# Kernel optimization log

Hardware: AMD Instinct MI355X
Metric: run time of the kernel (lower is better)

## Reference

```python
import jax, jax.numpy as jnp
import numpy as np
from jax import lax

H, H2, VJ, VC = 512, 256, 70, 2000
B, LIN, T = 64, 1024, 256
START = 1  # char2index['<s>']


def gru_step(h, x, Wih, Whh, bih, bhh):
    # PyTorch GRU cell math; gates ordered (r, z, n)
    gi = x @ Wih.T + bih
    gh = h @ Whh.T + bhh
    ir, iz, inn = jnp.split(gi, 3, axis=-1)
    hr, hz, hn = jnp.split(gh, 3, axis=-1)
    r = jax.nn.sigmoid(ir + hr)
    z = jax.nn.sigmoid(iz + hz)
    n = jnp.tanh(inn + r * hn)
    return (1.0 - z) * n + z * h


def setup_inputs() -> dict:
    key = jax.random.key(0)
    ks = jax.random.split(key, 24)
    u = lambda k, s: jax.random.uniform(k, s, jnp.float32, -0.1, 0.1)
    return {
        "input_tokens": jax.random.randint(ks[0], (B, LIN), 0, VJ),
        "target_tokens": jax.random.randint(ks[1], (B, T), 0, VC),
        "loss_mask": jnp.ones((B, T), jnp.float32),
        "emb_jamo": u(ks[2], (VJ, H)),
        "emb_char": u(ks[3], (VC, H)),
        "enc_Wih_f": u(ks[4], (3 * H2, H)),  "enc_Whh_f": u(ks[5], (3 * H2, H2)),
        "enc_bih_f": u(ks[6], (3 * H2,)),    "enc_bhh_f": u(ks[7], (3 * H2,)),
        "enc_Wih_b": u(ks[8], (3 * H2, H)),  "enc_Whh_b": u(ks[9], (3 * H2, H2)),
        "enc_bih_b": u(ks[10], (3 * H2,)),   "enc_bhh_b": u(ks[11], (3 * H2,)),
        "dec_Wih": u(ks[12], (3 * H, H)),    "dec_Whh": u(ks[13], (3 * H, H)),
        "dec_bih": u(ks[14], (3 * H,)),      "dec_bhh": u(ks[15], (3 * H,)),
        "attn_W": u(ks[16], (H, 2 * H)),     "attn_b": u(ks[17], (H,)),
        "comb_W": u(ks[18], (H, 2 * H)),     "comb_b": u(ks[19], (H,)),
        "out_W": u(ks[20], (VC, H)),         "out_b": u(ks[21], (VC,)),
    }


def reference(input_tokens, target_tokens, loss_mask, emb_jamo, emb_char,
              enc_Wih_f, enc_Whh_f, enc_bih_f, enc_bhh_f,
              enc_Wih_b, enc_Whh_b, enc_bih_b, enc_bhh_b,
              dec_Wih, dec_Whh, dec_bih, dec_bhh,
              attn_W, attn_b, comb_W, comb_b, out_W, out_b):
    b, lin = input_tokens.shape
    t_len = target_tokens.shape[1]
    h2 = enc_Whh_f.shape[1]

    # --- Encoder: step-by-step bidirectional GRU (per original Python loop,
    # both directions advance forward in time since seq_len=1 per call) ---
    xs = jnp.swapaxes(emb_jamo[input_tokens], 0, 1)  # [Lin, B, H]

    def enc_step(carry, xt):
        hf, hb = carry
        hf = gru_step(hf, xt, enc_Wih_f, enc_Whh_f, enc_bih_f, enc_bhh_f)
        hb = gru_step(hb, xt, enc_Wih_b, enc_Whh_b, enc_bih_b, enc_bhh_b)
        return (hf, hb), jnp.concatenate([hf, hb], axis=-1)

    init = (jnp.zeros((b, h2), xs.dtype), jnp.zeros((b, h2), xs.dtype))
    _, enc_out_t = lax.scan(enc_step, init, xs)      # [Lin, B, H]
    enc_out = jnp.swapaxes(enc_out_t, 0, 1)          # [B, Lin, H]
    h0 = enc_out_t[-1]                               # decoder init hidden [B, H]

    # --- Decoder: attention + GRU, greedy argmax feedback ---
    tok0 = jnp.full((b,), START, dtype=input_tokens.dtype)

    def dec_step(carry, _):
        tok, h = carry
        emb = emb_char[tok]                                           # [B, H]
        key_ = jnp.concatenate([emb, h], -1) @ attn_W.T + attn_b      # [B, H]
        scores = jnp.einsum('blh,bh->bl', enc_out, key_)              # [B, Lin]
        w = jax.nn.softmax(scores, axis=1)
        ctx = jnp.einsum('bl,blh->bh', w, enc_out)                    # [B, H]
        g = jax.nn.relu(jnp.concatenate([emb, ctx], -1) @ comb_W.T + comb_b)
        h_new = gru_step(h, g, dec_Wih, dec_Whh, dec_bih, dec_bhh)
        logp = jax.nn.log_softmax(h_new @ out_W.T + out_b, axis=-1)   # [B, VC]
        nxt = jnp.argmax(logp, axis=-1).astype(tok.dtype)
        return (nxt, h_new), (logp, w)

    _, (logps, ws) = lax.scan(dec_step, (tok0, h0), None, length=t_len)
    decoder_outputs = jnp.swapaxes(logps, 0, 1)       # [B, T, VC]
    decoder_attentions = jnp.transpose(ws, (1, 2, 0)) # [B, Lin, T]

    # NLLLoss(reduction='none') masked, mean over batch, summed over steps, /T
    nll = -jnp.take_along_axis(decoder_outputs, target_tokens[..., None], axis=-1)[..., 0]
    loss = jnp.sum(jnp.mean(nll * loss_mask, axis=0)) / t_len
    return decoder_outputs, decoder_attentions, loss
```

## Files before the change

### kernel.cpp

```cpp
#include <hip/hip_runtime.h>
#include <hip/hip_bf16.h>
#include <cstdint>
#include <cstddef>


#define DEV __device__ __forceinline__

constexpr int kH = 512, kH2 = 256, kVC = 2000, kB = 64, kLIN = 1024, kT = 256;
constexpr int kSTART = 1;

__global__ __launch_bounds__(256) void k_zero(float* p, int n) {
  int i = blockIdx.x * 256 + threadIdx.x;
  if (i < n) p[i] = 0.f;
}

__global__ __launch_bounds__(256)
void k_gi_table(const float* emb_jamo, const float* Wf, const float* Wb,
                const float* bihf, const float* bihb, float* gi) {
  int v = blockIdx.x >> 1, d = blockIdx.x & 1;
  const float* W = d ? Wb : Wf;
  const float* bih = d ? bihb : bihf;
  __shared__ float x[kH];
  for (int k = threadIdx.x; k < kH; k += 256) x[k] = emb_jamo[v * kH + k];
  __syncthreads();
  for (int j = threadIdx.x; j < 3 * kH2; j += 256) {
    float acc = bih[j];
    const float* row = W + (size_t)j * kH;
    for (int k = 0; k < kH; k += 4) {
      float4 f = *(const float4*)(row + k);
      acc += x[k] * f.x + x[k + 1] * f.y + x[k + 2] * f.z + x[k + 3] * f.w;
    }
    gi[(size_t)(v * 2 + d) * 768 + j] = acc;
  }
}

__global__ __launch_bounds__(256)
void k_ac_emb(const float* emb_char, const float* attn_W, const float* attn_b,
              const float* comb_W, const float* comb_b, float* A, float* C) {
  int v = blockIdx.x;
  __shared__ float x[kH];
  for (int k = threadIdx.x; k < kH; k += 256) x[k] = emb_char[v * kH + k];
  __syncthreads();
  for (int j = threadIdx.x; j < kH; j += 256) {
    float a = attn_b[j], c = comb_b[j];
    const float* ra = attn_W + (size_t)j * 1024;
    const float* rc = comb_W + (size_t)j * 1024;
    for (int k = 0; k < kH; k += 4) {
      float4 fa = *(const float4*)(ra + k), fc = *(const float4*)(rc + k);
      a += x[k] * fa.x + x[k + 1] * fa.y + x[k + 2] * fa.z + x[k + 3] * fa.w;
      c += x[k] * fc.x + x[k + 1] * fc.y + x[k + 2] * fc.z + x[k + 3] * fc.w;
    }
    A[(size_t)v * kH + j] = a;
    C[(size_t)v * kH + j] = c;
  }
}

__global__ __launch_bounds__(256)
void k_enc_step(const int* tokens, const float* Whf, const float* Whb,
                const float* bhhf, const float* bhhb, const float* gi,
                float* henc, float* enc, int t, int pp, int BC, int lbc, int b0) {
  int d = blockIdx.x >> lbc;
  int blk = blockIdx.x & (BC - 1);
  int b = threadIdx.x & (BC - 1), q = threadIdx.x >> lbc;
  int u = blk * (256 >> lbc) + q;
  const float* Whh = d ? Whb : Whf;
  const float* bhh = d ? bhhb : bhhf;
  const float* hin = henc + (size_t)(pp * 2 + d) * kH2 * BC;
  float* hout = henc + (size_t)((1 - pp) * 2 + d) * kH2 * BC;

  const float* wr = Whh + (size_t)(0 * kH2 + u) * kH2;
  const float* wz = Whh + (size_t)(1 * kH2 + u) * kH2;
  const float* wn = Whh + (size_t)(2 * kH2 + u) * kH2;
  float ar = bhh[u], az = bhh[kH2 + u], an = bhh[2 * kH2 + u];
  for (int k = 0; k < kH2; k += 4) {
    float4 fr = *(const float4*)(wr + k);
    float4 fz = *(const float4*)(wz + k);
    float4 fn = *(const float4*)(wn + k);
    float h0v = hin[(k + 0) * BC + b], h1v = hin[(k + 1) * BC + b];
    float h2v = hin[(k + 2) * BC + b], h3v = hin[(k + 3) * BC + b];
    ar += h0v * fr.x + h1v * fr.y + h2v * fr.z + h3v * fr.w;
    az += h0v * fz.x + h1v * fz.y + h2v * fz.z + h3v * fz.w;
    an += h0v * fn.x + h1v * fn.y + h2v * fn.z + h3v * fn.w;
  }
  int v = tokens[(size_t)(b0 + b) * kLIN + t];
  const float* git = gi + (size_t)(v * 2 + d) * 768;
  float r = 1.f / (1.f + expf(-(git[u] + ar)));
  float z = 1.f / (1.f + expf(-(git[kH2 + u] + az)));
  float n = tanhf(git[2 * kH2 + u] + r * an);
  float hprev = hin[u * BC + b];
  float hnew = (1.f - z) * n + z * hprev;
  hout[u * BC + b] = hnew;
  enc[((size_t)b * kLIN + t) * kH + d * kH2 + u] = hnew;
}

__global__ __launch_bounds__(256)
void k_prologue(const float* enc, const float* Atab, const float* aW,
                float* hr, float* ht, float* key, int* tok, int BC) {
  int b = blockIdx.x, tid = threadIdx.x;
  __shared__ float h[kH];
  const float* h0 = enc + ((size_t)b * kLIN + (kLIN - 1)) * kH;
  for (int k = tid; k < kH; k += 256) {
    float v = h0[k];
    h[k] = v;
    hr[(size_t)b * kH + k] = v;
    ht[(size_t)k * BC + b] = v;
  }
  if (tid == 0) tok[b] = kSTART;
  __syncthreads();
  const float* A = Atab + (size_t)kSTART * kH;
  for (int j = tid; j < kH; j += 256) {
    const float* row = aW + (size_t)j * 1024 + 512;
    float acc = A[j];
    for (int k = 0; k < kH; k += 4) {
      float4 f = *(const float4*)(row + k);
      acc += h[k] * f.x + h[k + 1] * f.y + h[k + 2] * f.z + h[k + 3] * f.w;
    }
    key[(size_t)b * kH + j] = acc;
  }
}

__global__ __launch_bounds__(256)
void k_scores(const float* encAll, const float* keyAll, float* sc,
              float* pm, float* pd, float* pctx) {
  int b = blockIdx.x >> 3, lt = blockIdx.x & 7;
  int tid = threadIdx.x, lane = tid & 63, w = tid >> 6, hl = lane & 31, half = lane >> 5;
  __shared__ float s_tile[128], e_tile[128], red[128];
  const float* enc = encAll + (size_t)b * kLIN * kH;
  float kreg[16];
  const float* key = keyAll + (size_t)b * kH + hl * 16;
#pragma unroll
  for (int m = 0; m < 16; m += 4) *(float4*)(kreg + m) = *(const float4*)(key + m);
  for (int i = 0; i < 16; i++) {
    int ll = w * 32 + i * 2 + half;
    int l = lt * 128 + ll;
    const float* row = enc + (size_t)l * kH + hl * 16;
    float acc = 0.f;
#pragma unroll
    for (int m = 0; m < 16; m += 4) {
      float4 v = *(const float4*)(row + m);
      acc += v.x * kreg[m] + v.y * kreg[m + 1] + v.z * kreg[m + 2] + v.w * kreg[m + 3];
    }
#pragma unroll
    for (int m2 = 16; m2 > 0; m2 >>= 1) acc += __shfl_xor(acc, m2, 32);
    if (hl == 0) { s_tile[ll] = acc; sc[(size_t)b * kLIN + l] = acc; }
  }
  __syncthreads();
  if (tid < 128) red[tid] = s_tile[tid];
  __syncthreads();
  for (int s = 64; s > 0; s >>= 1) {
    if (tid < s) red[tid] = fmaxf(red[tid], red[tid + s]);
    __syncthreads();
  }
  float mt = red[0];
  __syncthreads();
  if (tid < 128) { e_tile[tid] = expf(s_tile[tid] - mt); red[tid] = e_tile[tid]; }
  __syncthreads();
  for (int s = 64; s > 0; s >>= 1) {
    if (tid < s) red[tid] += red[tid + s];
    __syncthreads();
  }
  float dt = red[0];
  int h0i = tid * 2;
  float cx = 0.f, cy = 0.f;
  const float* base = enc + (size_t)(lt * 128) * kH + h0i;
  for (int l = 0; l < 128; l++) {
    float e = e_tile[l];
    float2 v = *(const float2*)(base + (size_t)l * kH);
    cx += e * v.x; cy += e * v.y;
  }
  float* pc = pctx + ((size_t)b * 8 + lt) * kH;
  pc[h0i] = cx; pc[h0i + 1] = cy;
  if (tid == 0) { pm[b * 8 + lt] = mt; pd[b * 8 + lt] = dt; }
}

__global__ __launch_bounds__(256)
void k_ctx_g(const float* cW, const float* Ctab, const float* sc,
             const float* pm, const float* pd, const float* pctx,
             const int* tok, float* out1, float* gt, int BC, int b0, int t) {
  int b = blockIdx.x, tid = threadIdx.x;
  __shared__ float f8[8], MD[2], ctxl[kH];
  __shared__ int tokl;
  if (tid == 0) {
    float M = -1e30f;
    for (int i = 0; i < 8; i++) M = fmaxf(M, pm[b * 8 + i]);
    float D = 0.f;
    for (int i = 0; i < 8; i++) {
      float f = expf(pm[b * 8 + i] - M);
      f8[i] = f; D += f * pd[b * 8 + i];
    }
    MD[0] = M; MD[1] = 1.f / D;
    tokl = tok[b];
  }
  __syncthreads();
  float M = MD[0], invD = MD[1];
  int h0i = tid * 2;
  float cx = 0.f, cy = 0.f;
  for (int i = 0; i < 8; i++) {
    const float* pc = pctx + ((size_t)b * 8 + i) * kH + h0i;
    cx += f8[i] * pc[0]; cy += f8[i] * pc[1];
  }
  ctxl[h0i] = cx * invD; ctxl[h0i + 1] = cy * invD;
  int gb = b0 + b;
  for (int l = tid; l < kLIN; l += 256)
    out1[((size_t)gb * kLIN + l) * kT + t] = expf(sc[(size_t)b * kLIN + l] - M) * invD;
  __syncthreads();
  int tk = tokl;
  for (int j = tid; j < kH; j += 256) {
    const float* row = cW + (size_t)j * 1024 + 512;
    float acc = Ctab[(size_t)tk * kH + j];
    for (int k = 0; k < kH; k += 4) {
      float4 f = *(const float4*)(row + k);
      acc += ctxl[k] * f.x + ctxl[k + 1] * f.y + ctxl[k + 2] * f.z + ctxl[k + 3] * f.w;
    }
    gt[(size_t)j * BC + b] = fmaxf(acc, 0.f);
  }
}

__global__ __launch_bounds__(256)
void k_gru(const float* Wih, const float* Whh, const float* bih, const float* bhh,
           const float* gt, float* ht, float* hr, int BC, int lbc, int pp) {
  int tid = threadIdx.x;
  int b = tid & (BC - 1), q = tid >> lbc;
  int u = blockIdx.x * (256 >> lbc) + q;
  const float* htp = ht + (size_t)pp * kH * BC;
  float air = bih[u], aiz = bih[kH + u], ain = bih[2 * kH + u];
  float ahr = bhh[u], ahz = bhh[kH + u], ahn = bhh[2 * kH + u];
  const float* wir = Wih + (size_t)(0 * kH + u) * kH;
  const float* wiz = Wih + (size_t)(1 * kH + u) * kH;
  const float* win = Wih + (size_t)(2 * kH + u) * kH;
  const float* whr = Whh + (size_t)(0 * kH + u) * kH;
  const float* whz = Whh + (size_t)(1 * kH + u) * kH;
  const float* whn = Whh + (size_t)(2 * kH + u) * kH;
  for (int k = 0; k < kH; k += 4) {
    float4 fir = *(const float4*)(wir + k), fiz = *(const float4*)(wiz + k), fin = *(const float4*)(win + k);
    float4 fhr = *(const float4*)(whr + k), fhz = *(const float4*)(whz + k), fhn = *(const float4*)(whn + k);
    float g0 = gt[(k + 0) * BC + b], g1 = gt[(k + 1) * BC + b];
    float g2 = gt[(k + 2) * BC + b], g3 = gt[(k + 3) * BC + b];
    float h0v = htp[(k + 0) * BC + b], h1v = htp[(k + 1) * BC + b];
    float h2v = htp[(k + 2) * BC + b], h3v = htp[(k + 3) * BC + b];
    air += g0 * fir.x + g1 * fir.y + g2 * fir.z + g3 * fir.w;
    aiz += g0 * fiz.x + g1 * fiz.y + g2 * fiz.z + g3 * fiz.w;
    ain += g0 * fin.x + g1 * fin.y + g2 * fin.z + g3 * fin.w;
    ahr += h0v * fhr.x + h1v * fhr.y + h2v * fhr.z + h3v * fhr.w;
    ahz += h0v * fhz.x + h1v * fhz.y + h2v * fhz.z + h3v * fhz.w;
    ahn += h0v * fhn.x + h1v * fhn.y + h2v * fhn.z + h3v * fhn.w;
  }
  float r = 1.f / (1.f + expf(-(air + ahr)));
  float z = 1.f / (1.f + expf(-(aiz + ahz)));
  float n = tanhf(ain + r * ahn);
  float hp = htp[(size_t)u * BC + b];
  float hnew = (1.f - z) * n + z * hp;
  ht[(size_t)(1 - pp) * kH * BC + (size_t)u * BC + b] = hnew;
  hr[(size_t)(1 - pp) * BC * kH + (size_t)b * kH + u] = hnew;
}

__global__ __launch_bounds__(256)
void k_logits(const float* oW, const float* ob, const float* hr, float* lg,
              int BC, int np) {
  int b = blockIdx.x >> 3, ct = blockIdx.x & 7;
  int tid = threadIdx.x, lane = tid & 63, w = tid >> 6, hl = lane & 31, half = lane >> 5;
  const float* hrow = hr + (size_t)np * BC * kH + (size_t)b * kH + hl * 16;
  float hreg[16];
#pragma unroll
  for (int m = 0; m < 16; m += 4) *(float4*)(hreg + m) = *(const float4*)(hrow + m);
  int c0 = ct * 250;
  for (int i = 0; i < 32; i++) {
    int c = c0 + i * 8 + w * 2 + half;
    if (c < c0 + 250) {
      const float* row = oW + (size_t)c * kH + hl * 16;
      float acc = 0.f;
#pragma unroll
      for (int m = 0; m < 16; m += 4) {
        float4 v = *(const float4*)(row + m);
        acc += v.x * hreg[m] + v.y * hreg[m + 1] + v.z * hreg[m + 2] + v.w * hreg[m + 3];
      }
#pragma unroll
      for (int m2 = 16; m2 > 0; m2 >>= 1) acc += __shfl_xor(acc, m2, 32);
      if (hl == 0) lg[(size_t)b * kVC + c] = acc + ob[c];
    }
  }
}

__global__ __launch_bounds__(256)
void k_finish(const float* aW, const int* targets, const float* mask,
              const float* Atab, const float* hr, const float* lg,
              float* key, int* tok, float* loss, float* out0,
              int BC, int b0, int t, int np) {
  int b = blockIdx.x, tid = threadIdx.x, gb = b0 + b;
  __shared__ float rv[256]; __shared__ int ri[256]; __shared__ float rs[256];
  __shared__ float hsh[kH];
  const float* lrow = lg + (size_t)b * kVC;
  float xv[8];
  float bv = -3.4e38f; int bi = kVC;
#pragma unroll
  for (int i = 0; i < 8; i++) {
    int c = tid + i * 256;
    float x = (c < kVC) ? lrow[c] : -3.4e38f;
    xv[i] = x;
    if (x > bv) { bv = x; bi = c; }
  }
  rv[tid] = bv; ri[tid] = bi;
  __syncthreads();
  for (int s = 128; s > 0; s >>= 1) {
    if (tid < s) {
      float v2 = rv[tid + s]; int i2 = ri[tid + s];
      if (v2 > rv[tid] || (v2 == rv[tid] && i2 < ri[tid])) { rv[tid] = v2; ri[tid] = i2; }
    }
    __syncthreads();
  }
  float M = rv[0]; int nt = ri[0];
  float se = 0.f;
#pragma unroll
  for (int i = 0; i < 8; i++) { int c = tid + i * 256; if (c < kVC) se += expf(xv[i] - M); }
  rs[tid] = se;
  __syncthreads();
  for (int s = 128; s > 0; s >>= 1) {
    if (tid < s) rs[tid] += rs[tid + s];
    __syncthreads();
  }
  float lse = M + logf(rs[0]);
  float* orow = out0 + ((size_t)gb * kT + t) * kVC;
#pragma unroll
  for (int i = 0; i < 8; i++) { int c = tid + i * 256; if (c < kVC) orow[c] = xv[i] - lse; }
  if (tid == 0) {
    tok[b] = nt;
    int tg = targets[(size_t)gb * kT + t];
    float mk = mask[(size_t)gb * kT + t];
    atomicAdd(loss, (lse - lrow[tg]) * mk * (1.f / 16384.f));
  }
  const float* hrow = hr + (size_t)np * BC * kH + (size_t)b * kH;
  for (int k = tid; k < kH; k += 256) hsh[k] = hrow[k];
  __syncthreads();
  const float* A = Atab + (size_t)nt * kH;
  for (int j = tid; j < kH; j += 256) {
    const float* row = aW + (size_t)j * 1024 + 512;
    float acc = A[j];
    for (int k = 0; k < kH; k += 4) {
      float4 f = *(const float4*)(row + k);
      acc += hsh[k] * f.x + hsh[k + 1] * f.y + hsh[k + 2] * f.z + hsh[k + 3] * f.w;
    }
    key[(size_t)b * kH + j] = acc;
  }
}

__global__ void k_loss_out(float* dst, const float* loss) {
  if (threadIdx.x == 0 && blockIdx.x == 0) *dst = *loss;
}

extern "C" void kernel_launch(void* const* d_in, const int* in_sizes, int n_in,
                              void* d_out, int out_size, void* d_ws, size_t ws_size,
                              hipStream_t stream) {
  (void)in_sizes; (void)n_in;
  const int*   tok_in = (const int*)d_in[0];
  const int*   tgt    = (const int*)d_in[1];
  const float* mask   = (const float*)d_in[2];
  const float* emb_j  = (const float*)d_in[3];
  const float* emb_c  = (const float*)d_in[4];
  const float* eWif   = (const float*)d_in[5];
  const float* eWhf   = (const float*)d_in[6];
  const float* ebif   = (const float*)d_in[7];
  const float* ebhf   = (const float*)d_in[8];
  const float* eWib   = (const float*)d_in[9];
  const float* eWhb   = (const float*)d_in[10];
  const float* ebib   = (const float*)d_in[11];
  const float* ebhb   = (const float*)d_in[12];
  const float* dWi    = (const float*)d_in[13];
  const float* dWh    = (const float*)d_in[14];
  const float* dbi    = (const float*)d_in[15];
  const float* dbh    = (const float*)d_in[16];
  const float* aW     = (const float*)d_in[17];
  const float* ab     = (const float*)d_in[18];
  const float* cW     = (const float*)d_in[19];
  const float* cb     = (const float*)d_in[20];
  const float* oW     = (const float*)d_in[21];
  const float* ob     = (const float*)d_in[22];
  float* ws   = (float*)d_ws;
  float* out0 = (float*)d_out;
  float* out1 = out0 + (size_t)kB * kT * kVC;

  const size_t GI = 0;
  const size_t A  = GI + 107520;
  const size_t C  = A + 1024000;
  const size_t SMALL = C + 1024000;
  size_t o = SMALL;
  const size_t HENC = o; o += 4 * 256 * 64;
  const size_t KEY  = o; o += 64 * 512;
  const size_t SC   = o; o += 64 * 1024;
  const size_t PM   = o; o += 512;
  const size_t PD   = o; o += 512;
  const size_t PCT  = o; o += 64 * 8 * 512;
  const size_t GT   = o; o += 512 * 64;
  const size_t HR   = o; o += 2 * 64 * 512;
  const size_t HT   = o; o += 2 * 512 * 64;
  const size_t LG   = o; o += 64 * 2000;
  const size_t TOKo = o; o += 64;
  const size_t LOSS = o; o += 1;
  const size_t ENC  = o;
  const int small_n = (int)(ENC - SMALL);

  int BC = 64;
  while (BC > 8 && (ENC + (size_t)BC * kLIN * kH) * sizeof(float) > ws_size) BC >>= 1;
  int lbc = (BC == 64) ? 6 : (BC == 32) ? 5 : (BC == 16) ? 4 : 3;
  int NC = kB / BC;
  int* tokp = (int*)(ws + TOKo);

  k_zero<<<(small_n + 255) / 256, 256, 0, stream>>>(ws + SMALL, small_n);
  k_gi_table<<<140, 256, 0, stream>>>(emb_j, eWif, eWib, ebif, ebib, ws + GI);
  k_ac_emb<<<2000, 256, 0, stream>>>(emb_c, aW, ab, cW, cb, ws + A, ws + C);

  for (int c = 0; c < NC; c++) {
    int b0 = c * BC;
    k_zero<<<(4 * 256 * BC + 255) / 256, 256, 0, stream>>>(ws + HENC, 4 * 256 * BC);
    for (int t = 0; t < kLIN; t++)
      k_enc_step<<<2 * BC, 256, 0, stream>>>(tok_in, eWhf, eWhb, ebhf, ebhb,
                                             ws + GI, ws + HENC, ws + ENC,
                                             t, t & 1, BC, lbc, b0);
    k_prologue<<<BC, 256, 0, stream>>>(ws + ENC, ws + A, aW, ws + HR, ws + HT,
                                       ws + KEY, tokp, BC);
    for (int t = 0; t < kT; t++) {
      int pp = t & 1, np = 1 - pp;
      k_scores<<<BC * 8, 256, 0, stream>>>(ws + ENC, ws + KEY, ws + SC,
                                           ws + PM, ws + PD, ws + PCT);
      k_ctx_g<<<BC, 256, 0, stream>>>(cW, ws + C, ws + SC, ws + PM, ws + PD,
                                      ws + PCT, tokp, out1, ws + GT, BC, b0, t);
      k_gru<<<2 * BC, 256, 0, stream>>>(dWi, dWh, dbi, dbh, ws + GT,
                                        ws + HT, ws + HR, BC, lbc, pp);
      k_logits<<<BC * 8, 256, 0, stream>>>(oW, ob, ws + HR, ws + LG, BC, np);
      k_finish<<<BC, 256, 0, stream>>>(aW, tgt, mask, ws + A, ws + HR, ws + LG,
                                       ws + KEY, tokp, ws + LOSS, out0,
                                       BC, b0, t, np);
    }
  }
  k_loss_out<<<1, 64, 0, stream>>>(out0 + (size_t)out_size - 1, ws + LOSS);
}
```

Baseline: 62.72 ms.

## Fuse encoder and decoder time loops into persistent per-sequence kernels

The per-timestep launches (1024 encoder steps plus 5 kernels per decoder step) are replaced by two persistent kernels. The encoder runs one block per sequence and direction, looping over time with its hidden state in shared memory. The decoder runs one 1024-thread block per sequence that does scores, context, GRU, logits, log-softmax and key update inside the block. This removes thousands of launches and the global round-trips for intermediates. In exchange it uses far fewer blocks (only 2*BC or BC), so each block re-streams the weight matrices on its own and parallelism per step drops.

```diff
diff --git a/kernel.cpp b/kernel.cpp
--- a/kernel.cpp
+++ b/kernel.cpp
@@ -1,10 +1,7 @@
 #include <hip/hip_runtime.h>
-#include <hip/hip_bf16.h>
 #include <cstdint>
 #include <cstddef>
 
-
-#define DEV __device__ __forceinline__
 
 constexpr int kH = 512, kH2 = 256, kVC = 2000, kB = 64, kLIN = 1024, kT = 256;
 constexpr int kSTART = 1;
@@ -56,290 +53,308 @@
 }
 
 __global__ __launch_bounds__(256)
-void k_enc_step(const int* tokens, const float* Whf, const float* Whb,
-                const float* bhhf, const float* bhhb, const float* gi,
-                float* henc, float* enc, int t, int pp, int BC, int lbc, int b0) {
-  int d = blockIdx.x >> lbc;
-  int blk = blockIdx.x & (BC - 1);
-  int b = threadIdx.x & (BC - 1), q = threadIdx.x >> lbc;
-  int u = blk * (256 >> lbc) + q;
+void k_enc_pb(const int* tokens, const float* Whf, const float* Whb,
+              const float* bhhf, const float* bhhb, const float* gi,
+              float* enc, int b0) {
+  int b = blockIdx.x >> 1, d = blockIdx.x & 1;
+  int u = threadIdx.x;
   const float* Whh = d ? Whb : Whf;
   const float* bhh = d ? bhhb : bhhf;
-  const float* hin = henc + (size_t)(pp * 2 + d) * kH2 * BC;
-  float* hout = henc + (size_t)((1 - pp) * 2 + d) * kH2 * BC;
-
+  __shared__ float hsh[kH2];
+  hsh[u] = 0.f;
+  __syncthreads();
   const float* wr = Whh + (size_t)(0 * kH2 + u) * kH2;
   const float* wz = Whh + (size_t)(1 * kH2 + u) * kH2;
   const float* wn = Whh + (size_t)(2 * kH2 + u) * kH2;
-  float ar = bhh[u], az = bhh[kH2 + u], an = bhh[2 * kH2 + u];
-  for (int k = 0; k < kH2; k += 4) {
-    float4 fr = *(const float4*)(wr + k);
-    float4 fz = *(const float4*)(wz + k);
-    float4 fn = *(const float4*)(wn + k);
-    float h0v = hin[(k + 0) * BC + b], h1v = hin[(k + 1) * BC + b];
-    float h2v = hin[(k + 2) * BC + b], h3v = hin[(k + 3) * BC + b];
-    ar += h0v * fr.x + h1v * fr.y + h2v * fr.z + h3v * fr.w;
-    az += h0v * fz.x + h1v * fz.y + h2v * fz.z + h3v * fz.w;
-    an += h0v * fn.x + h1v * fn.y + h2v * fn.z + h3v * fn.w;
-  }
-  int v = tokens[(size_t)(b0 + b) * kLIN + t];
-  const float* git = gi + (size_t)(v * 2 + d) * 768;
-  float r = 1.f / (1.f + expf(-(git[u] + ar)));
-  float z = 1.f / (1.f + expf(-(git[kH2 + u] + az)));
-  float n = tanhf(git[2 * kH2 + u] + r * an);
-  float hprev = hin[u * BC + b];
-  float hnew = (1.f - z) * n + z * hprev;
-  hout[u * BC + b] = hnew;
-  enc[((size_t)b * kLIN + t) * kH + d * kH2 + u] = hnew;
-}
-
-__global__ __launch_bounds__(256)
-void k_prologue(const float* enc, const float* Atab, const float* aW,
-                float* hr, float* ht, float* key, int* tok, int BC) {
-  int b = blockIdx.x, tid = threadIdx.x;
-  __shared__ float h[kH];
-  const float* h0 = enc + ((size_t)b * kLIN + (kLIN - 1)) * kH;
-  for (int k = tid; k < kH; k += 256) {
-    float v = h0[k];
-    h[k] = v;
-    hr[(size_t)b * kH + k] = v;
-    ht[(size_t)k * BC + b] = v;
-  }
-  if (tid == 0) tok[b] = kSTART;
+  float br = bhh[u], bz = bhh[kH2 + u], bn = bhh[2 * kH2 + u];
+  const int* myTok = tokens + (size_t)(b0 + b) * kLIN;
+  float* encCol = enc + (size_t)b * kLIN * kH + d * kH2 + u;
+  for (int t = 0; t < kLIN; ++t) {
+    float ar = br, az = bz, an = bn;
+    for (int k = 0; k < kH2; k += 4) {
+      float4 fr = *(const float4*)(wr + k);
+      float4 fz = *(const float4*)(wz + k);
+      float4 fn = *(const float4*)(wn + k);
+      float h0v = hsh[k], h1v = hsh[k + 1], h2v = hsh[k + 2], h3v = hsh[k + 3];
+      ar += h0v * fr.x + h1v * fr.y + h2v * fr.z + h3v * fr.w;
+      az += h0v * fz.x + h1v * fz.y + h2v * fz.z + h3v * fz.w;
+      an += h0v * fn.x + h1v * fn.y + h2v * fn.z + h3v * fn.w;
+    }
+    int v = myTok[t];
+    const float* git = gi + (size_t)(v * 2 + d) * 768;
+    float r = 1.f / (1.f + expf(-(git[u] + ar)));
+    float z = 1.f / (1.f + expf(-(git[kH2 + u] + az)));
+    float n = tanhf(git[2 * kH2 + u] + r * an);
+    float hprev = hsh[u];
+    float hnew = (1.f - z) * n + z * hprev;
+    __syncthreads();
+    hsh[u] = hnew;
+    encCol[(size_t)t * kH] = hnew;
+    __syncthreads();
+  }
+}
+
+__global__ __launch_bounds__(1024, 1)
+void k_dec_pb(const float* encAll, const float* cW, const float* Ctab,
+              const float* dWi, const float* dWh, const float* dbi, const float* dbh,
+              const float* oW, const float* ob, const float* aW, const float* Atab,
+              const int* targets, const float* maskp,
+              float* loss, float* out0, float* out1, int b0) {
+  int b = blockIdx.x;
+  int tid = threadIdx.x;
+  int sg = tid >> 8, stid = tid & 255;
+  int lane = stid & 63, w = stid >> 6, hl = lane & 31, half = lane >> 5;
+
+  __shared__ float s_tile[4][128], e_tile[4][128], red[4][128];
+  __shared__ float pm_s[8], pd_s[8];
+  __shared__ float pctx_s[8][kH];
+  __shared__ __align__(16) float sc_all[kLIN];
+  __shared__ __align__(16) float key_s[kH];
+  __shared__ __align__(16) float hbuf[2][kH];
+  __shared__ __align__(16) float ctxl[kH];
+  __shared__ __align__(16) float gt_s[kH];
+  __shared__ float lg_s[kVC];
+  __shared__ float rv[256]; __shared__ int ri[256]; __shared__ float rs[256];
+  __shared__ float MD[2]; __shared__ float f8[8];
+  __shared__ int tok_s;
+
+  const float* encB = encAll + (size_t)b * kLIN * kH;
+  int gb = b0 + b;
+
+  for (int k = tid; k < kH; k += 1024) hbuf[0][k] = encB[(size_t)(kLIN - 1) * kH + k];
+  if (tid == 0) tok_s = kSTART;
   __syncthreads();
-  const float* A = Atab + (size_t)kSTART * kH;
-  for (int j = tid; j < kH; j += 256) {
+  if (tid < kH) {
+    int j = tid;
     const float* row = aW + (size_t)j * 1024 + 512;
-    float acc = A[j];
+    float acc = Atab[(size_t)kSTART * kH + j];
     for (int k = 0; k < kH; k += 4) {
       float4 f = *(const float4*)(row + k);
-      acc += h[k] * f.x + h[k + 1] * f.y + h[k + 2] * f.z + h[k + 3] * f.w;
-    }
-    key[(size_t)b * kH + j] = acc;
-  }
-}
-
-__global__ __launch_bounds__(256)
-void k_scores(const float* encAll, const float* keyAll, float* sc,
-              float* pm, float* pd, float* pctx) {
-  int b = blockIdx.x >> 3, lt = blockIdx.x & 7;
-  int tid = threadIdx.x, lane = tid & 63, w = tid >> 6, hl = lane & 31, half = lane >> 5;
-  __shared__ float s_tile[128], e_tile[128], red[128];
-  const float* enc = encAll + (size_t)b * kLIN * kH;
-  float kreg[16];
-  const float* key = keyAll + (size_t)b * kH + hl * 16;
-#pragma unroll
-  for (int m = 0; m < 16; m += 4) *(float4*)(kreg + m) = *(const float4*)(key + m);
-  for (int i = 0; i < 16; i++) {
-    int ll = w * 32 + i * 2 + half;
-    int l = lt * 128 + ll;
-    const float* row = enc + (size_t)l * kH + hl * 16;
-    float acc = 0.f;
-#pragma unroll
-    for (int m = 0; m < 16; m += 4) {
-      float4 v = *(const float4*)(row + m);
-      acc += v.x * kreg[m] + v.y * kreg[m + 1] + v.z * kreg[m + 2] + v.w * kreg[m + 3];
-    }
-#pragma unroll
-    for (int m2 = 16; m2 > 0; m2 >>= 1) acc += __shfl_xor(acc, m2, 32);
-    if (hl == 0) { s_tile[ll] = acc; sc[(size_t)b * kLIN + l] = acc; }
+      acc += hbuf[0][k] * f.x + hbuf[0][k + 1] * f.y + hbuf[0][k + 2] * f.z + hbuf[0][k + 3] * f.w;
+    }
+    key_s[j] = acc;
   }
   __syncthreads();
-  if (tid < 128) red[tid] = s_tile[tid];
-  __syncthreads();
-  for (int s = 64; s > 0; s >>= 1) {
-    if (tid < s) red[tid] = fmaxf(red[tid], red[tid + s]);
-    __syncthreads();
-  }
-  float mt = red[0];
-  __syncthreads();
-  if (tid < 128) { e_tile[tid] = expf(s_tile[tid] - mt); red[tid] = e_tile[tid]; }
-  __syncthreads();
-  for (int s = 64; s > 0; s >>= 1) {
-    if (tid < s) red[tid] += red[tid + s];
-    __syncthreads();
-  }
-  float dt = red[0];
-  int h0i = tid * 2;
-  float cx = 0.f, cy = 0.f;
-  const float* base = enc + (size_t)(lt * 128) * kH + h0i;
-  for (int l = 0; l < 128; l++) {
-    float e = e_tile[l];
-    float2 v = *(const float2*)(base + (size_t)l * kH);
-    cx += e * v.x; cy += e * v.y;
-  }
-  float* pc = pctx + ((size_t)b * 8 + lt) * kH;
-  pc[h0i] = cx; pc[h0i + 1] = cy;
-  if (tid == 0) { pm[b * 8 + lt] = mt; pd[b * 8 + lt] = dt; }
-}
-
-__global__ __launch_bounds__(256)
-void k_ctx_g(const float* cW, const float* Ctab, const float* sc,
-             const float* pm, const float* pd, const float* pctx,
-             const int* tok, float* out1, float* gt, int BC, int b0, int t) {
-  int b = blockIdx.x, tid = threadIdx.x;
-  __shared__ float f8[8], MD[2], ctxl[kH];
-  __shared__ int tokl;
-  if (tid == 0) {
-    float M = -1e30f;
-    for (int i = 0; i < 8; i++) M = fmaxf(M, pm[b * 8 + i]);
-    float D = 0.f;
-    for (int i = 0; i < 8; i++) {
-      float f = expf(pm[b * 8 + i] - M);
-      f8[i] = f; D += f * pd[b * 8 + i];
-    }
-    MD[0] = M; MD[1] = 1.f / D;
-    tokl = tok[b];
-  }
-  __syncthreads();
-  float M = MD[0], invD = MD[1];
-  int h0i = tid * 2;
-  float cx = 0.f, cy = 0.f;
-  for (int i = 0; i < 8; i++) {
-    const float* pc = pctx + ((size_t)b * 8 + i) * kH + h0i;
-    cx += f8[i] * pc[0]; cy += f8[i] * pc[1];
-  }
-  ctxl[h0i] = cx * invD; ctxl[h0i + 1] = cy * invD;
-  int gb = b0 + b;
-  for (int l = tid; l < kLIN; l += 256)
-    out1[((size_t)gb * kLIN + l) * kT + t] = expf(sc[(size_t)b * kLIN + l] - M) * invD;
-  __syncthreads();
-  int tk = tokl;
-  for (int j = tid; j < kH; j += 256) {
-    const float* row = cW + (size_t)j * 1024 + 512;
-    float acc = Ctab[(size_t)tk * kH + j];
-    for (int k = 0; k < kH; k += 4) {
-      float4 f = *(const float4*)(row + k);
-      acc += ctxl[k] * f.x + ctxl[k + 1] * f.y + ctxl[k + 2] * f.z + ctxl[k + 3] * f.w;
-    }
-    gt[(size_t)j * BC + b] = fmaxf(acc, 0.f);
-  }
-}
-
-__global__ __launch_bounds__(256)
-void k_gru(const float* Wih, const float* Whh, const float* bih, const float* bhh,
-           const float* gt, float* ht, float* hr, int BC, int lbc, int pp) {
-  int tid = threadIdx.x;
-  int b = tid & (BC - 1), q = tid >> lbc;
-  int u = blockIdx.x * (256 >> lbc) + q;
-  const float* htp = ht + (size_t)pp * kH * BC;
-  float air = bih[u], aiz = bih[kH + u], ain = bih[2 * kH + u];
-  float ahr = bhh[u], ahz = bhh[kH + u], ahn = bhh[2 * kH + u];
-  const float* wir = Wih + (size_t)(0 * kH + u) * kH;
-  const float* wiz = Wih + (size_t)(1 * kH + u) * kH;
-  const float* win = Wih + (size_t)(2 * kH + u) * kH;
-  const float* whr = Whh + (size_t)(0 * kH + u) * kH;
-  const float* whz = Whh + (size_t)(1 * kH + u) * kH;
-  const float* whn = Whh + (size_t)(2 * kH + u) * kH;
-  for (int k = 0; k < kH; k += 4) {
-    float4 fir = *(const float4*)(wir + k), fiz = *(const float4*)(wiz + k), fin = *(const float4*)(win + k);
-    float4 fhr = *(const float4*)(whr + k), fhz = *(const float4*)(whz + k), fhn = *(const float4*)(whn + k);
-    float g0 = gt[(k + 0) * BC + b], g1 = gt[(k + 1) * BC + b];
-    float g2 = gt[(k + 2) * BC + b], g3 = gt[(k + 3) * BC + b];
-    float h0v = htp[(k + 0) * BC + b], h1v = htp[(k + 1) * BC + b];
-    float h2v = htp[(k + 2) * BC + b], h3v = htp[(k + 3) * BC + b];
-    air += g0 * fir.x + g1 * fir.y + g2 * fir.z + g3 * fir.w;
-    aiz += g0 * fiz.x + g1 * fiz.y + g2 * fiz.z + g3 * fiz.w;
-    ain += g0 * fin.x + g1 * fin.y + g2 * fin.z + g3 * fin.w;
-    ahr += h0v * fhr.x + h1v * fhr.y + h2v * fhr.z + h3v * fhr.w;
-    ahz += h0v * fhz.x + h1v * fhz.y + h2v * fhz.z + h3v * fhz.w;
-    ahn += h0v * fhn.x + h1v * fhn.y + h2v * fhn.z + h3v * fhn.w;
-  }
-  float r = 1.f / (1.f + expf(-(air + ahr)));
-  float z = 1.f / (1.f + expf(-(aiz + ahz)));
-  float n = tanhf(ain + r * ahn);
-  float hp = htp[(size_t)u * BC + b];
-  float hnew = (1.f - z) * n + z * hp;
-  ht[(size_t)(1 - pp) * kH * BC + (size_t)u * BC + b] = hnew;
-  hr[(size_t)(1 - pp) * BC * kH + (size_t)b * kH + u] = hnew;
-}
-
-__global__ __launch_bounds__(256)
-void k_logits(const float* oW, const float* ob, const float* hr, float* lg,
-              int BC, int np) {
-  int b = blockIdx.x >> 3, ct = blockIdx.x & 7;
-  int tid = threadIdx.x, lane = tid & 63, w = tid >> 6, hl = lane & 31, half = lane >> 5;
-  const float* hrow = hr + (size_t)np * BC * kH + (size_t)b * kH + hl * 16;
-  float hreg[16];
-#pragma unroll
-  for (int m = 0; m < 16; m += 4) *(float4*)(hreg + m) = *(const float4*)(hrow + m);
-  int c0 = ct * 250;
-  for (int i = 0; i < 32; i++) {
-    int c = c0 + i * 8 + w * 2 + half;
-    if (c < c0 + 250) {
-      const float* row = oW + (size_t)c * kH + hl * 16;
-      float acc = 0.f;
-#pragma unroll
-      for (int m = 0; m < 16; m += 4) {
-        float4 v = *(const float4*)(row + m);
-        acc += v.x * hreg[m] + v.y * hreg[m + 1] + v.z * hreg[m + 2] + v.w * hreg[m + 3];
-      }
-#pragma unroll
-      for (int m2 = 16; m2 > 0; m2 >>= 1) acc += __shfl_xor(acc, m2, 32);
-      if (hl == 0) lg[(size_t)b * kVC + c] = acc + ob[c];
-    }
-  }
-}
-
-__global__ __launch_bounds__(256)
-void k_finish(const float* aW, const int* targets, const float* mask,
-              const float* Atab, const float* hr, const float* lg,
-              float* key, int* tok, float* loss, float* out0,
-              int BC, int b0, int t, int np) {
-  int b = blockIdx.x, tid = threadIdx.x, gb = b0 + b;
-  __shared__ float rv[256]; __shared__ int ri[256]; __shared__ float rs[256];
-  __shared__ float hsh[kH];
-  const float* lrow = lg + (size_t)b * kVC;
-  float xv[8];
-  float bv = -3.4e38f; int bi = kVC;
-#pragma unroll
-  for (int i = 0; i < 8; i++) {
-    int c = tid + i * 256;
-    float x = (c < kVC) ? lrow[c] : -3.4e38f;
-    xv[i] = x;
-    if (x > bv) { bv = x; bi = c; }
-  }
-  rv[tid] = bv; ri[tid] = bi;
-  __syncthreads();
-  for (int s = 128; s > 0; s >>= 1) {
-    if (tid < s) {
-      float v2 = rv[tid + s]; int i2 = ri[tid + s];
-      if (v2 > rv[tid] || (v2 == rv[tid] && i2 < ri[tid])) { rv[tid] = v2; ri[tid] = i2; }
-    }
-    __syncthreads();
-  }
-  float M = rv[0]; int nt = ri[0];
-  float se = 0.f;
-#pragma unroll
-  for (int i = 0; i < 8; i++) { int c = tid + i * 256; if (c < kVC) se += expf(xv[i] - M); }
-  rs[tid] = se;
-  __syncthreads();
-  for (int s = 128; s > 0; s >>= 1) {
-    if (tid < s) rs[tid] += rs[tid + s];
-    __syncthreads();
-  }
-  float lse = M + logf(rs[0]);
-  float* orow = out0 + ((size_t)gb * kT + t) * kVC;
-#pragma unroll
-  for (int i = 0; i < 8; i++) { int c = tid + i * 256; if (c < kVC) orow[c] = xv[i] - lse; }
-  if (tid == 0) {
-    tok[b] = nt;
-    int tg = targets[(size_t)gb * kT + t];
-    float mk = mask[(size_t)gb * kT + t];
-    atomicAdd(loss, (lse - lrow[tg]) * mk * (1.f / 16384.f));
-  }
-  const float* hrow = hr + (size_t)np * BC * kH + (size_t)b * kH;
-  for (int k = tid; k < kH; k += 256) hsh[k] = hrow[k];
-  __syncthreads();
-  const float* A = Atab + (size_t)nt * kH;
-  for (int j = tid; j < kH; j += 256) {
-    const float* row = aW + (size_t)j * 1024 + 512;
-    float acc = A[j];
-    for (int k = 0; k < kH; k += 4) {
-      float4 f = *(const float4*)(row + k);
-      acc += hsh[k] * f.x + hsh[k + 1] * f.y + hsh[k + 2] * f.z + hsh[k + 3] * f.w;
-    }
-    key[(size_t)b * kH + j] = acc;
+
+  for (int t = 0; t < kT; ++t) {
+    int pp = t & 1;
+    const float* hprev = hbuf[pp];
+    float* hnew = hbuf[1 - pp];
+
+    float kreg[16];
+#pragma unroll
+    for (int m = 0; m < 16; m += 4) *(float4*)(kreg + m) = *(const float4*)(key_s + hl * 16 + m);
+    for (int r = 0; r < 2; ++r) {
+      int lt = sg + r * 4;
+      for (int i0 = 0; i0 < 16; i0 += 2) {
+        float4 v[2][4];
+#pragma unroll
+        for (int j = 0; j < 2; j++) {
+          int ll = w * 32 + (i0 + j) * 2 + half;
+          const float* row = encB + (size_t)(lt * 128 + ll) * kH + hl * 16;
+#pragma unroll
+          for (int m = 0; m < 4; m++) v[j][m] = *(const float4*)(row + m * 4);
+        }
+#pragma unroll
+        for (int j = 0; j < 2; j++) {
+          int ll = w * 32 + (i0 + j) * 2 + half;
+          float acc = 0.f;
+#pragma unroll
+          for (int m = 0; m < 4; m++)
+            acc += v[j][m].x * kreg[4 * m] + v[j][m].y * kreg[4 * m + 1] +
+                   v[j][m].z * kreg[4 * m + 2] + v[j][m].w * kreg[4 * m + 3];
+#pragma unroll
+          for (int m2 = 16; m2 > 0; m2 >>= 1) acc += __shfl_xor(acc, m2, 32);
+          if (hl == 0) { s_tile[sg][ll] = acc; sc_all[lt * 128 + ll] = acc; }
+        }
+      }
+      __syncthreads();
+      if (stid < 128) red[sg][stid] = s_tile[sg][stid];
+      __syncthreads();
+      for (int s = 64; s > 0; s >>= 1) {
+        if (stid < s) red[sg][stid] = fmaxf(red[sg][stid], red[sg][stid + s]);
+        __syncthreads();
+      }
+      float mt = red[sg][0];
+      __syncthreads();
+      if (stid < 128) { e_tile[sg][stid] = expf(s_tile[sg][stid] - mt); red[sg][stid] = e_tile[sg][stid]; }
+      __syncthreads();
+      for (int s = 64; s > 0; s >>= 1) {
+        if (stid < s) red[sg][stid] += red[sg][stid + s];
+        __syncthreads();
+      }
+      float dt = red[sg][0];
+      int h0i = stid * 2;
+      float cx = 0.f, cy = 0.f;
+      const float* base = encB + (size_t)(lt * 128) * kH + h0i;
+      for (int l0 = 0; l0 < 128; l0 += 4) {
+        float2 v0 = *(const float2*)(base + (size_t)(l0 + 0) * kH);
+        float2 v1 = *(const float2*)(base + (size_t)(l0 + 1) * kH);
+        float2 v2 = *(const float2*)(base + (size_t)(l0 + 2) * kH);
+        float2 v3 = *(const float2*)(base + (size_t)(l0 + 3) * kH);
+        float e0 = e_tile[sg][l0], e1 = e_tile[sg][l0 + 1];
+        float e2 = e_tile[sg][l0 + 2], e3 = e_tile[sg][l0 + 3];
+        cx += e0 * v0.x; cy += e0 * v0.y;
+        cx += e1 * v1.x; cy += e1 * v1.y;
+        cx += e2 * v2.x; cy += e2 * v2.y;
+        cx += e3 * v3.x; cy += e3 * v3.y;
+      }
+      pctx_s[lt][h0i] = cx; pctx_s[lt][h0i + 1] = cy;
+      if (stid == 0) { pm_s[lt] = mt; pd_s[lt] = dt; }
+      __syncthreads();
+    }
+
+    if (tid == 0) {
+      float M = -1e30f;
+      for (int i = 0; i < 8; i++) M = fmaxf(M, pm_s[i]);
+      float D = 0.f;
+      for (int i = 0; i < 8; i++) {
+        float f = expf(pm_s[i] - M);
+        f8[i] = f; D += f * pd_s[i];
+      }
+      MD[0] = M; MD[1] = 1.f / D;
+    }
+    __syncthreads();
+    float M = MD[0], invD = MD[1];
+    if (tid < 256) {
+      int h0i = tid * 2;
+      float cx = 0.f, cy = 0.f;
+      for (int i = 0; i < 8; i++) { cx += f8[i] * pctx_s[i][h0i]; cy += f8[i] * pctx_s[i][h0i + 1]; }
+      ctxl[h0i] = cx * invD; ctxl[h0i + 1] = cy * invD;
+    }
+    out1[((size_t)gb * kLIN + tid) * kT + t] = expf(sc_all[tid] - M) * invD;
+    __syncthreads();
+    if (tid < kH) {
+      int j = tid, tk = tok_s;
+      const float* row = cW + (size_t)j * 1024 + 512;
+      float acc = Ctab[(size_t)tk * kH + j];
+      for (int k = 0; k < kH; k += 4) {
+        float4 f = *(const float4*)(row + k);
+        acc += ctxl[k] * f.x + ctxl[k + 1] * f.y + ctxl[k + 2] * f.z + ctxl[k + 3] * f.w;
+      }
+      gt_s[j] = fmaxf(acc, 0.f);
+    }
+    __syncthreads();
+
+    if (tid < kH) {
+      int u = tid;
+      float air = dbi[u], aiz = dbi[kH + u], ain = dbi[2 * kH + u];
+      float ahr = dbh[u], ahz = dbh[kH + u], ahn = dbh[2 * kH + u];
+      const float* wir = dWi + (size_t)(0 * kH + u) * kH;
+      const float* wiz = dWi + (size_t)(1 * kH + u) * kH;
+      const float* win = dWi + (size_t)(2 * kH + u) * kH;
+      const float* whr = dWh + (size_t)(0 * kH + u) * kH;
+      const float* whz = dWh + (size_t)(1 * kH + u) * kH;
+      const float* whn = dWh + (size_t)(2 * kH + u) * kH;
+      for (int k = 0; k < kH; k += 4) {
+        float4 fir = *(const float4*)(wir + k), fiz = *(const float4*)(wiz + k), fin = *(const float4*)(win + k);
+        float4 fhr = *(const float4*)(whr + k), fhz = *(const float4*)(whz + k), fhn = *(const float4*)(whn + k);
+        float g0 = gt_s[k], g1 = gt_s[k + 1], g2 = gt_s[k + 2], g3 = gt_s[k + 3];
+        float h0v = hprev[k], h1v = hprev[k + 1], h2v = hprev[k + 2], h3v = hprev[k + 3];
+        air += g0 * fir.x + g1 * fir.y + g2 * fir.z + g3 * fir.w;
+        aiz += g0 * fiz.x + g1 * fiz.y + g2 * fiz.z + g3 * fiz.w;
+        ain += g0 * fin.x + g1 * fin.y + g2 * fin.z + g3 * fin.w;
+        ahr += h0v * fhr.x + h1v * fhr.y + h2v * fhr.z + h3v * fhr.w;
+        ahz += h0v * fhz.x + h1v * fhz.y + h2v * fhz.z + h3v * fhz.w;
+        ahn += h0v * fhn.x + h1v * fhn.y + h2v * fhn.z + h3v * fhn.w;
+      }
+      float rr = 1.f / (1.f + expf(-(air + ahr)));
+      float zz = 1.f / (1.f + expf(-(aiz + ahz)));
+      float nn = tanhf(ain + rr * ahn);
+      float hp = hprev[u];
+      hnew[u] = (1.f - zz) * nn + zz * hp;
+    }
+    __syncthreads();
+
+    {
+      float hreg[16];
+#pragma unroll
+      for (int m = 0; m < 16; m += 4) *(float4*)(hreg + m) = *(const float4*)(&hnew[hl * 16 + m]);
+      for (int r = 0; r < 2; ++r) {
+        int ct = sg + r * 4;
+        int c0 = ct * 250;
+        for (int i0 = 0; i0 < 32; i0 += 2) {
+          int ca = c0 + (i0 + 0) * 8 + w * 2 + half;
+          int cb = c0 + (i0 + 1) * 8 + w * 2 + half;
+          int cca = ca < kVC ? ca : kVC - 1;
+          int ccb = cb < kVC ? cb : kVC - 1;
+          float4 va[4], vb[4];
+          const float* rowa = oW + (size_t)cca * kH + hl * 16;
+          const float* rowb = oW + (size_t)ccb * kH + hl * 16;
+#pragma unroll
+          for (int m = 0; m < 4; m++) { va[m] = *(const float4*)(rowa + m * 4); vb[m] = *(const float4*)(rowb + m * 4); }
+          float acca = 0.f, accb = 0.f;
+#pragma unroll
+          for (int m = 0; m < 4; m++)
+            acca += va[m].x * hreg[4 * m] + va[m].y * hreg[4 * m + 1] +
+                    va[m].z * hreg[4 * m + 2] + va[m].w * hreg[4 * m + 3];
+#pragma unroll
+          for (int m = 0; m < 4; m++)
+            accb += vb[m].x * hreg[4 * m] + vb[m].y * hreg[4 * m + 1] +
+                    vb[m].z * hreg[4 * m + 2] + vb[m].w * hreg[4 * m + 3];
+#pragma unroll
+          for (int m2 = 16; m2 > 0; m2 >>= 1) acca += __shfl_xor(acca, m2, 32);
+#pragma unroll
+          for (int m2 = 16; m2 > 0; m2 >>= 1) accb += __shfl_xor(accb, m2, 32);
+          if (ca < c0 + 250 && hl == 0) lg_s[ca] = acca + ob[ca];
+          if (cb < c0 + 250 && hl == 0) lg_s[cb] = accb + ob[cb];
+        }
+      }
+    }
+    __syncthreads();
+
+    float xv[8];
+    if (sg == 0) {
+      float bv = -3.4e38f; int bi = kVC;
+#pragma unroll
+      for (int i = 0; i < 8; i++) {
+        int c = stid + i * 256;
+        float x = (c < kVC) ? lg_s[c] : -3.4e38f;
+        xv[i] = x;
+        if (x > bv) { bv = x; bi = c; }
+      }
+      rv[stid] = bv; ri[stid] = bi;
+    }
+    __syncthreads();
+    for (int s = 128; s > 0; s >>= 1) {
+      if (sg == 0 && stid < s) {
+        float v2 = rv[stid + s]; int i2 = ri[stid + s];
+        if (v2 > rv[stid] || (v2 == rv[stid] && i2 < ri[stid])) { rv[stid] = v2; ri[stid] = i2; }
+      }
+      __syncthreads();
+    }
+    float Me = rv[0]; int nt = ri[0];
+    if (sg == 0) {
+      float se = 0.f;
+#pragma unroll
+      for (int i = 0; i < 8; i++) { int c = stid + i * 256; if (c < kVC) se += expf(xv[i] - Me); }
+      rs[stid] = se;
+    }
+    __syncthreads();
+    for (int s = 128; s > 0; s >>= 1) {
+      if (sg == 0 && stid < s) rs[stid] += rs[stid + s];
+      __syncthreads();
+    }
+    float lse = Me + logf(rs[0]);
+    for (int c = tid; c < kVC; c += 1024)
+      out0[((size_t)gb * kT + t) * kVC + c] = lg_s[c] - lse;
+    if (tid == 0) {
+      tok_s = nt;
+      int tg = targets[(size_t)gb * kT + t];
+      float mk = maskp[(size_t)gb * kT + t];
+      atomicAdd(loss, (lse - lg_s[tg]) * mk * (1.f / 16384.f));
+    }
+    if (tid < kH) {
+      int j = tid;
+      const float* row = aW + (size_t)j * 1024 + 512;
+      float acc = Atab[(size_t)nt * kH + j];
+      for (int k = 0; k < kH; k += 4) {
+        float4 f = *(const float4*)(row + k);
+        acc += hnew[k] * f.x + hnew[k + 1] * f.y + hnew[k + 2] * f.z + hnew[k + 3] * f.w;
+      }
+      key_s[j] = acc;
+    }
+    __syncthreads();
   }
 }
 
@@ -378,58 +393,33 @@
   float* out0 = (float*)d_out;
   float* out1 = out0 + (size_t)kB * kT * kVC;
 
-  const size_t GI = 0;
-  const size_t A  = GI + 107520;
-  const size_t C  = A + 1024000;
-  const size_t SMALL = C + 1024000;
-  size_t o = SMALL;
-  const size_t HENC = o; o += 4 * 256 * 64;
-  const size_t KEY  = o; o += 64 * 512;
-  const size_t SC   = o; o += 64 * 1024;
-  const size_t PM   = o; o += 512;
-  const size_t PD   = o; o += 512;
-  const size_t PCT  = o; o += 64 * 8 * 512;
-  const size_t GT   = o; o += 512 * 64;
-  const size_t HR   = o; o += 2 * 64 * 512;
-  const size_t HT   = o; o += 2 * 512 * 64;
-  const size_t LG   = o; o += 64 * 2000;
-  const size_t TOKo = o; o += 64;
-  const size_t LOSS = o; o += 1;
-  const size_t ENC  = o;
-  const int small_n = (int)(ENC - SMALL);
+  const size_t GI   = 0;
+  const size_t A    = GI + 107520;
+  const size_t C    = A + 1024000;
+  const size_t LOSS = C + 1024000;
+  const size_t ENC  = LOSS + 1;
 
   int BC = 64;
   while (BC > 8 && (ENC + (size_t)BC * kLIN * kH) * sizeof(float) > ws_size) BC >>= 1;
-  int lbc = (BC == 64) ? 6 : (BC == 32) ? 5 : (BC == 16) ? 4 : 3;
   int NC = kB / BC;
-  int* tokp = (int*)(ws + TOKo);
-
-  k_zero<<<(small_n + 255) / 256, 256, 0, stream>>>(ws + SMALL, small_n);
-  k_gi_table<<<140, 256, 0, stream>>>(emb_j, eWif, eWib, ebif, ebib, ws + GI);
-  k_ac_emb<<<2000, 256, 0, stream>>>(emb_c, aW, ab, cW, cb, ws + A, ws + C);
+
+  float* gi_p   = ws + GI;
+  float* A_p    = ws + A;
+  float* C_p    = ws + C;
+  float* loss_p = ws + LOSS;
+  float* enc_p  = ws + ENC;
+
+  k_zero<<<1, 256, 0, stream>>>(loss_p, 1);
+  k_gi_table<<<140, 256, 0, stream>>>(emb_j, eWif, eWib, ebif, ebib, gi_p);
+  k_ac_emb<<<2000, 256, 0, stream>>>(emb_c, aW, ab, cW, cb, A_p, C_p);
 
   for (int c = 0; c < NC; c++) {
     int b0 = c * BC;
-    k_zero<<<(4 * 256 * BC + 255) / 256, 256, 0, stream>>>(ws + HENC, 4 * 256 * BC);
-    for (int t = 0; t < kLIN; t++)
-      k_enc_step<<<2 * BC, 256, 0, stream>>>(tok_in, eWhf, eWhb, ebhf, ebhb,
-                                             ws + GI, ws + HENC, ws + ENC,
-                                             t, t & 1, BC, lbc, b0);
-    k_prologue<<<BC, 256, 0, stream>>>(ws + ENC, ws + A, aW, ws + HR, ws + HT,
-                                       ws + KEY, tokp, BC);
-    for (int t = 0; t < kT; t++) {
-      int pp = t & 1, np = 1 - pp;
-      k_scores<<<BC * 8, 256, 0, stream>>>(ws + ENC, ws + KEY, ws + SC,
-                                           ws + PM, ws + PD, ws + PCT);
-      k_ctx_g<<<BC, 256, 0, stream>>>(cW, ws + C, ws + SC, ws + PM, ws + PD,
-                                      ws + PCT, tokp, out1, ws + GT, BC, b0, t);
-      k_gru<<<2 * BC, 256, 0, stream>>>(dWi, dWh, dbi, dbh, ws + GT,
-                                        ws + HT, ws + HR, BC, lbc, pp);
-      k_logits<<<BC * 8, 256, 0, stream>>>(oW, ob, ws + HR, ws + LG, BC, np);
-      k_finish<<<BC, 256, 0, stream>>>(aW, tgt, mask, ws + A, ws + HR, ws + LG,
-                                       ws + KEY, tokp, ws + LOSS, out0,
-                                       BC, b0, t, np);
-    }
-  }
-  k_loss_out<<<1, 64, 0, stream>>>(out0 + (size_t)out_size - 1, ws + LOSS);
-}
+    k_enc_pb<<<2 * BC, 256, 0, stream>>>(tok_in, eWhf, eWhb, ebhf, ebhb,
+                                         gi_p, enc_p, b0);
+    k_dec_pb<<<BC, 1024, 0, stream>>>(enc_p, cW, C_p, dWi, dWh, dbi, dbh,
+                                      oW, ob, aW, A_p, tgt, mask,
+                                      loss_p, out0, out1, b0);
+  }
+  k_loss_out<<<1, 64, 0, stream>>>(out0 + (size_t)out_size - 1, loss_p);
+}
```

New measurement: 120.6 ms. +92.3%, slower.

## Fuse encoder time loop into one persistent kernel per batch-direction

Applied to the files above, without the earlier changes.

Replaces 1024 per-timestep encoder launches with a single kernel where each block owns one batch element and direction, keeps the hidden state in shared memory, and loops over time with barriers. This removes kernel launch and global hidden-state round-trip overhead. In exchange, recurrent weights are no longer shared across batch elements within a block, so each block re-reads the full weight matrix from cache every step.

```diff
diff --git a/kernel.cpp b/kernel.cpp
--- a/kernel.cpp
+++ b/kernel.cpp
@@ -1,10 +1,7 @@
 #include <hip/hip_runtime.h>
-#include <hip/hip_bf16.h>
 #include <cstdint>
 #include <cstddef>
 
-
-#define DEV __device__ __forceinline__
 
 constexpr int kH = 512, kH2 = 256, kVC = 2000, kB = 64, kLIN = 1024, kT = 256;
 constexpr int kSTART = 1;
@@ -56,41 +53,45 @@
 }
 
 __global__ __launch_bounds__(256)
-void k_enc_step(const int* tokens, const float* Whf, const float* Whb,
-                const float* bhhf, const float* bhhb, const float* gi,
-                float* henc, float* enc, int t, int pp, int BC, int lbc, int b0) {
-  int d = blockIdx.x >> lbc;
-  int blk = blockIdx.x & (BC - 1);
-  int b = threadIdx.x & (BC - 1), q = threadIdx.x >> lbc;
-  int u = blk * (256 >> lbc) + q;
+void k_enc_pb(const int* tokens, const float* Whf, const float* Whb,
+              const float* bhhf, const float* bhhb, const float* gi,
+              float* enc, int b0) {
+  int b = blockIdx.x >> 1, d = blockIdx.x & 1;
+  int u = threadIdx.x;
   const float* Whh = d ? Whb : Whf;
   const float* bhh = d ? bhhb : bhhf;
-  const float* hin = henc + (size_t)(pp * 2 + d) * kH2 * BC;
-  float* hout = henc + (size_t)((1 - pp) * 2 + d) * kH2 * BC;
-
+  __shared__ float hsh[kH2];
+  hsh[u] = 0.f;
+  __syncthreads();
   const float* wr = Whh + (size_t)(0 * kH2 + u) * kH2;
   const float* wz = Whh + (size_t)(1 * kH2 + u) * kH2;
   const float* wn = Whh + (size_t)(2 * kH2 + u) * kH2;
-  float ar = bhh[u], az = bhh[kH2 + u], an = bhh[2 * kH2 + u];
-  for (int k = 0; k < kH2; k += 4) {
-    float4 fr = *(const float4*)(wr + k);
-    float4 fz = *(const float4*)(wz + k);
-    float4 fn = *(const float4*)(wn + k);
-    float h0v = hin[(k + 0) * BC + b], h1v = hin[(k + 1) * BC + b];
-    float h2v = hin[(k + 2) * BC + b], h3v = hin[(k + 3) * BC + b];
-    ar += h0v * fr.x + h1v * fr.y + h2v * fr.z + h3v * fr.w;
-    az += h0v * fz.x + h1v * fz.y + h2v * fz.z + h3v * fz.w;
-    an += h0v * fn.x + h1v * fn.y + h2v * fn.z + h3v * fn.w;
-  }
-  int v = tokens[(size_t)(b0 + b) * kLIN + t];
-  const float* git = gi + (size_t)(v * 2 + d) * 768;
-  float r = 1.f / (1.f + expf(-(git[u] + ar)));
-  float z = 1.f / (1.f + expf(-(git[kH2 + u] + az)));
-  float n = tanhf(git[2 * kH2 + u] + r * an);
-  float hprev = hin[u * BC + b];
-  float hnew = (1.f - z) * n + z * hprev;
-  hout[u * BC + b] = hnew;
-  enc[((size_t)b * kLIN + t) * kH + d * kH2 + u] = hnew;
+  float br = bhh[u], bz = bhh[kH2 + u], bn = bhh[2 * kH2 + u];
+  const int* myTok = tokens + (size_t)(b0 + b) * kLIN;
+  float* encCol = enc + (size_t)b * kLIN * kH + d * kH2 + u;
+  for (int t = 0; t < kLIN; ++t) {
+    float ar = br, az = bz, an = bn;
+    for (int k = 0; k < kH2; k += 4) {
+      float4 fr = *(const float4*)(wr + k);
+      float4 fz = *(const float4*)(wz + k);
+      float4 fn = *(const float4*)(wn + k);
+      float h0v = hsh[k], h1v = hsh[k + 1], h2v = hsh[k + 2], h3v = hsh[k + 3];
+      ar += h0v * fr.x + h1v * fr.y + h2v * fr.z + h3v * fr.w;
+      az += h0v * fz.x + h1v * fz.y + h2v * fz.z + h3v * fz.w;
+      an += h0v * fn.x + h1v * fn.y + h2v * fn.z + h3v * fn.w;
+    }
+    int v = myTok[t];
+    const float* git = gi + (size_t)(v * 2 + d) * 768;
+    float r = 1.f / (1.f + expf(-(git[u] + ar)));
+    float z = 1.f / (1.f + expf(-(git[kH2 + u] + az)));
+    float n = tanhf(git[2 * kH2 + u] + r * an);
+    float hprev = hsh[u];
+    float hnew = (1.f - z) * n + z * hprev;
+    __syncthreads();
+    hsh[u] = hnew;
+    encCol[(size_t)t * kH] = hnew;
+    __syncthreads();
+  }
 }
 
 __global__ __launch_bounds__(256)
@@ -383,7 +384,6 @@
   const size_t C  = A + 1024000;
   const size_t SMALL = C + 1024000;
   size_t o = SMALL;
-  const size_t HENC = o; o += 4 * 256 * 64;
   const size_t KEY  = o; o += 64 * 512;
   const size_t SC   = o; o += 64 * 1024;
   const size_t PM   = o; o += 512;
@@ -404,32 +404,42 @@
   int NC = kB / BC;
   int* tokp = (int*)(ws + TOKo);
 
+  float* gi_p   = ws + GI;
+  float* A_p    = ws + A;
+  float* C_p    = ws + C;
+  float* key_p  = ws + KEY;
+  float* sc_p   = ws + SC;
+  float* pm_p   = ws + PM;
+  float* pd_p   = ws + PD;
+  float* pct_p  = ws + PCT;
+  float* gt_p   = ws + GT;
+  float* hr_p   = ws + HR;
+  float* ht_p   = ws + HT;
+  float* lg_p   = ws + LG;
+  float* loss_p = ws + LOSS;
+  float* enc_p  = ws + ENC;
+
   k_zero<<<(small_n + 255) / 256, 256, 0, stream>>>(ws + SMALL, small_n);
-  k_gi_table<<<140, 256, 0, stream>>>(emb_j, eWif, eWib, ebif, ebib, ws + GI);
-  k_ac_emb<<<2000, 256, 0, stream>>>(emb_c, aW, ab, cW, cb, ws + A, ws + C);
+  k_gi_table<<<140, 256, 0, stream>>>(emb_j, eWif, eWib, ebif, ebib, gi_p);
+  k_ac_emb<<<2000, 256, 0, stream>>>(emb_c, aW, ab, cW, cb, A_p, C_p);
 
   for (int c = 0; c < NC; c++) {
     int b0 = c * BC;
-    k_zero<<<(4 * 256 * BC + 255) / 256, 256, 0, stream>>>(ws + HENC, 4 * 256 * BC);
-    for (int t = 0; t < kLIN; t++)
-      k_enc_step<<<2 * BC, 256, 0, stream>>>(tok_in, eWhf, eWhb, ebhf, ebhb,
-                                             ws + GI, ws + HENC, ws + ENC,
-                                             t, t & 1, BC, lbc, b0);
-    k_prologue<<<BC, 256, 0, stream>>>(ws + ENC, ws + A, aW, ws + HR, ws + HT,
-                                       ws + KEY, tokp, BC);
+    k_enc_pb<<<2 * BC, 256, 0, stream>>>(tok_in, eWhf, eWhb, ebhf, ebhb,
+                                         gi_p, enc_p, b0);
+    k_prologue<<<BC, 256, 0, stream>>>(enc_p, A_p, aW, hr_p, ht_p, key_p, tokp, BC);
     for (int t = 0; t < kT; t++) {
       int pp = t & 1, np = 1 - pp;
-      k_scores<<<BC * 8, 256, 0, stream>>>(ws + ENC, ws + KEY, ws + SC,
-                                           ws + PM, ws + PD, ws + PCT);
-      k_ctx_g<<<BC, 256, 0, stream>>>(cW, ws + C, ws + SC, ws + PM, ws + PD,
-                                      ws + PCT, tokp, out1, ws + GT, BC, b0, t);
-      k_gru<<<2 * BC, 256, 0, stream>>>(dWi, dWh, dbi, dbh, ws + GT,
-                                        ws + HT, ws + HR, BC, lbc, pp);
-      k_logits<<<BC * 8, 256, 0, stream>>>(oW, ob, ws + HR, ws + LG, BC, np);
-      k_finish<<<BC, 256, 0, stream>>>(aW, tgt, mask, ws + A, ws + HR, ws + LG,
-                                       ws + KEY, tokp, ws + LOSS, out0,
+      k_scores<<<BC * 8, 256, 0, stream>>>(enc_p, key_p, sc_p, pm_p, pd_p, pct_p);
+      k_ctx_g<<<BC, 256, 0, stream>>>(cW, C_p, sc_p, pm_p, pd_p, pct_p,
+                                      tokp, out1, gt_p, BC, b0, t);
+      k_gru<<<2 * BC, 256, 0, stream>>>(dWi, dWh, dbi, dbh, gt_p,
+                                        ht_p, hr_p, BC, lbc, pp);
+      k_logits<<<BC * 8, 256, 0, stream>>>(oW, ob, hr_p, lg_p, BC, np);
+      k_finish<<<BC, 256, 0, stream>>>(aW, tgt, mask, A_p, hr_p, lg_p,
+                                       key_p, tokp, loss_p, out0,
                                        BC, b0, t, np);
     }
   }
-  k_loss_out<<<1, 64, 0, stream>>>(out0 + (size_t)out_size - 1, ws + LOSS);
-}
+  k_loss_out<<<1, 64, 0, stream>>>(out0 + (size_t)out_size - 1, loss_p);
+}
```

Result: slower. 73.91 ms (+17.8%).
